# Optimization experiments

Hardware: AMD Instinct MI355X
Metric: run time of the kernel (lower is better)

## Reference

```python
import jax, jax.numpy as jnp
import numpy as np

N_NODES = 50000
D_IN = 128
D_OUT = 128
N_EDGES = 800000


def setup_inputs() -> dict:
    key = jax.random.key(0)
    k1, k2, k3, k4 = jax.random.split(key, 4)
    x = jax.random.normal(k1, (N_NODES, D_IN), dtype=jnp.float32)
    # nn.Linear(input_size, output_size, bias=False): weight is [out, in], y = x @ W.T.
    # We store W1 as [in, out] so y = x @ W1 (same math, transposed storage).
    W1 = jax.random.normal(k2, (D_IN, D_OUT), dtype=jnp.float32) * (1.0 / np.sqrt(D_IN))
    row = jax.random.randint(k3, (N_EDGES,), 0, N_NODES, dtype=jnp.int64)
    col = jax.random.randint(k4, (N_EDGES,), 0, N_NODES, dtype=jnp.int64)
    edge_index = jnp.stack([row, col], axis=0)  # [2, E]
    return {"x": x, "W1": W1, "edge_index": edge_index}


def reference(x, W1, edge_index):
    # Linear transform: [N, D_in] @ [D_in, D_out] -> [N, D_out]
    norm_m = x @ W1
    adj_row = edge_index[0]  # source nodes (gather)
    adj_col = edge_index[1]  # destination nodes (scatter)
    gathered = norm_m[adj_row]  # [E, D_out]
    pooled = jax.ops.segment_max(gathered, adj_col, num_segments=x.shape[0])
    # torch_scatter fills segments with no incoming edges with 0 (not -inf)
    deg = jax.ops.segment_sum(jnp.ones_like(adj_col, dtype=jnp.int32), adj_col,
                              num_segments=x.shape[0])
    pooled = jnp.where((deg > 0)[:, None], pooled, jnp.zeros_like(pooled))
    return jnp.concatenate((x, pooled), axis=1)  # [N, D_in + D_out]
```

## Files before the change

### kernel.cpp

```cpp
#include <hip/hip_runtime.h>


#define N_DIN 128
#define CAP 64

typedef __attribute__((ext_vector_type(8))) short bf16x8;
typedef __attribute__((ext_vector_type(4))) float f32x4;

__device__ __forceinline__ short f32_bf16(float f) {
    unsigned u = __float_as_uint(f);
    return (short)((u + 0x7fffu + ((u >> 16) & 1u)) >> 16);
}

__global__ __launch_bounds__(256) void wconv(const float* __restrict__ W,
                                             short* __restrict__ Wt) {
    int i = blockIdx.x * 256 + threadIdx.x;
    int k = i >> 5, n0 = (i & 31) * 4;
    float4 v = *(const float4*)(W + k * 128 + n0);
    Wt[(n0 + 0) * 128 + k] = f32_bf16(v.x);
    Wt[(n0 + 1) * 128 + k] = f32_bf16(v.y);
    Wt[(n0 + 2) * 128 + k] = f32_bf16(v.z);
    Wt[(n0 + 3) * 128 + k] = f32_bf16(v.w);
}

__global__ __launch_bounds__(256) void fused_gemm_scatter(
        const float* __restrict__ X, const short* __restrict__ Wt,
        short* __restrict__ Yb, float* __restrict__ out, int N, int gblocks,
        const int* __restrict__ row, const int* __restrict__ col,
        int* __restrict__ cur, unsigned short* __restrict__ csrc, int E) {
    if ((int)blockIdx.x >= gblocks) {
        int e = ((int)blockIdx.x - gblocks) * 256 + (int)threadIdx.x;
        if (e < E) {
            int dst = col[e];
            int pos = atomicAdd(&cur[dst], 1);
            if (pos < CAP)
                csrc[dst * CAP + pos] = (unsigned short)row[e];
        }
        return;
    }
    __shared__ short c_lds[4][32][128];
    const int tid = threadIdx.x;
    const int w = tid >> 6, l = tid & 63;
    const int lr = l & 15, lg = l >> 4;
    const int R0 = (int)blockIdx.x * 128 + w * 32;

    bf16x8 af[2][4];
#pragma unroll
    for (int rt = 0; rt < 2; ++rt) {
        int gr = R0 + rt * 16 + lr;
        int grc = gr < N ? gr : N - 1;
#pragma unroll
        for (int t = 0; t < 4; ++t) {
            int kc = t * 32 + lg * 8;
            float4 v0 = *(const float4*)(X + (size_t)grc * 128 + kc);
            float4 v1 = *(const float4*)(X + (size_t)grc * 128 + kc + 4);
            if (gr < N) {
                *(float4*)(out + (size_t)gr * 256 + kc)     = v0;
                *(float4*)(out + (size_t)gr * 256 + kc + 4) = v1;
            }
            bf16x8 a;
            a[0] = f32_bf16(v0.x); a[1] = f32_bf16(v0.y);
            a[2] = f32_bf16(v0.z); a[3] = f32_bf16(v0.w);
            a[4] = f32_bf16(v1.x); a[5] = f32_bf16(v1.y);
            a[6] = f32_bf16(v1.z); a[7] = f32_bf16(v1.w);
            af[rt][t] = a;
        }
    }
#pragma unroll
    for (int ct = 0; ct < 8; ++ct) {
        f32x4 c0 = {0.f, 0.f, 0.f, 0.f}, c1 = {0.f, 0.f, 0.f, 0.f};
        const short* bp = Wt + (ct * 16 + lr) * 128;
#pragma unroll
        for (int t = 0; t < 4; ++t) {
            bf16x8 b = *(const bf16x8*)(bp + t * 32 + lg * 8);
            c0 = __builtin_amdgcn_mfma_f32_16x16x32_bf16(af[0][t], b, c0, 0, 0, 0);
            c1 = __builtin_amdgcn_mfma_f32_16x16x32_bf16(af[1][t], b, c1, 0, 0, 0);
        }
#pragma unroll
        for (int i = 0; i < 4; ++i) {
            c_lds[w][lg * 4 + i][ct * 16 + lr]      = f32_bf16(c0[i]);
            c_lds[w][16 + lg * 4 + i][ct * 16 + lr] = f32_bf16(c1[i]);
        }
    }
#pragma unroll
    for (int it = 0; it < 8; ++it) {
        int cid = it * 64 + l;
        int r2 = cid >> 4, c2 = cid & 15;
        int gr = R0 + r2;
        if (gr < N) {
            bf16x8 vv = *(const bf16x8*)(&c_lds[w][r2][c2 * 8]);
            *(bf16x8*)(Yb + (size_t)gr * 128 + c2 * 8) = vv;
        }
    }
}

__global__ __launch_bounds__(256) void pool_bf16(const unsigned* __restrict__ nmb,
                                                 const int* __restrict__ cur,
                                                 const unsigned short* __restrict__ csrc,
                                                 float* __restrict__ out, int N) {
    int node = blockIdx.x * 4 + (threadIdx.x >> 6);
    if (node >= N) return;
    int lane = threadIdx.x & 63;
    int deg = cur[node];
    if (deg > CAP) deg = CAP;
    const unsigned short* lst = csrc + node * CAP;
    float2 acc = make_float2(-INFINITY, -INFINITY);
    int j = 0;
    for (; j + 4 <= deg; j += 4) {
        int s0 = lst[j], s1 = lst[j + 1], s2 = lst[j + 2], s3 = lst[j + 3];
        unsigned v0 = nmb[s0 * 64 + lane];
        unsigned v1 = nmb[s1 * 64 + lane];
        unsigned v2 = nmb[s2 * 64 + lane];
        unsigned v3 = nmb[s3 * 64 + lane];
        acc.x = fmaxf(acc.x, fmaxf(fmaxf(__uint_as_float(v0 << 16), __uint_as_float(v1 << 16)),
                                   fmaxf(__uint_as_float(v2 << 16), __uint_as_float(v3 << 16))));
        acc.y = fmaxf(acc.y, fmaxf(fmaxf(__uint_as_float(v0 & 0xffff0000u), __uint_as_float(v1 & 0xffff0000u)),
                                   fmaxf(__uint_as_float(v2 & 0xffff0000u), __uint_as_float(v3 & 0xffff0000u))));
    }
    for (; j < deg; ++j) {
        unsigned v0 = nmb[lst[j] * 64 + lane];
        acc.x = fmaxf(acc.x, __uint_as_float(v0 << 16));
        acc.y = fmaxf(acc.y, __uint_as_float(v0 & 0xffff0000u));
    }
    if (deg == 0) acc = make_float2(0.f, 0.f);
    *(float2*)(out + (size_t)node * 256 + N_DIN + lane * 2) = acc;
}

extern "C" void kernel_launch(void* const* d_in, const int* in_sizes, int n_in,
                              void* d_out, int out_size, void* d_ws, size_t ws_size,
                              hipStream_t stream) {
    const float* x  = (const float*)d_in[0];
    const float* W1 = (const float*)d_in[1];
    const int* ei   = (const int*)d_in[2];
    const int N = in_sizes[0] / N_DIN;
    const int E = in_sizes[2] / 2;
    const int* row = ei;
    const int* col = ei + E;
    float* out = (float*)d_out;

    short* norm_mb = (short*)d_ws;
    short* Wt = norm_mb + (size_t)N * N_DIN;
    int* cur  = (int*)(Wt + 128 * 128);
    unsigned short* csrc = (unsigned short*)(cur + N);

    const int gblocks = (N + 127) / 128;
    const int sblocks = (E + 255) / 256;

    hipMemsetAsync(cur, 0, (size_t)N * sizeof(int), stream);
    wconv<<<16, 256, 0, stream>>>(W1, Wt);
    fused_gemm_scatter<<<gblocks + sblocks, 256, 0, stream>>>(
        x, Wt, norm_mb, out, N, gblocks, row, col, cur, csrc, E);
    pool_bf16<<<(N + 3) / 4, 256, 0, stream>>>((const unsigned*)norm_mb, cur, csrc, out, N);
}
```

Before: 168.6 us.

## Merge memset, weight convert, GEMM/scatter and pooling into one cooperative kernel

Replaces the memset plus three kernel launches with a single persistent cooperative kernel. Grid-wide syncs separate the weight conversion and counter clearing, the GEMM/edge-bucketing phase, and the max-pooling phase. The aim is to remove launch gaps and inter-kernel drain between stages. In exchange, a persistent grid sized by occupancy replaces the many small blocks, adds grid-barrier cost, and keeps the original multi-kernel path as a fallback if the cooperative launch fails.

```diff
diff --git a/kernel.cpp b/kernel.cpp
--- a/kernel.cpp
+++ b/kernel.cpp
@@ -1,4 +1,7 @@
 #include <hip/hip_runtime.h>
+#include <hip/hip_cooperative_groups.h>
+
+namespace cg = cooperative_groups;
 
 
 #define N_DIN 128
@@ -12,9 +15,8 @@
     return (short)((u + 0x7fffu + ((u >> 16) & 1u)) >> 16);
 }
 
-__global__ __launch_bounds__(256) void wconv(const float* __restrict__ W,
-                                             short* __restrict__ Wt) {
-    int i = blockIdx.x * 256 + threadIdx.x;
+__device__ __forceinline__ void wconv_unit(int i, const float* __restrict__ W,
+                                           short* __restrict__ Wt) {
     int k = i >> 5, n0 = (i & 31) * 4;
     float4 v = *(const float4*)(W + k * 128 + n0);
     Wt[(n0 + 0) * 128 + k] = f32_bf16(v.x);
@@ -23,26 +25,14 @@
     Wt[(n0 + 3) * 128 + k] = f32_bf16(v.w);
 }
 
-__global__ __launch_bounds__(256) void fused_gemm_scatter(
-        const float* __restrict__ X, const short* __restrict__ Wt,
-        short* __restrict__ Yb, float* __restrict__ out, int N, int gblocks,
-        const int* __restrict__ row, const int* __restrict__ col,
-        int* __restrict__ cur, unsigned short* __restrict__ csrc, int E) {
-    if ((int)blockIdx.x >= gblocks) {
-        int e = ((int)blockIdx.x - gblocks) * 256 + (int)threadIdx.x;
-        if (e < E) {
-            int dst = col[e];
-            int pos = atomicAdd(&cur[dst], 1);
-            if (pos < CAP)
-                csrc[dst * CAP + pos] = (unsigned short)row[e];
-        }
-        return;
-    }
-    __shared__ short c_lds[4][32][128];
-    const int tid = threadIdx.x;
+__device__ __forceinline__ void gemm_tile(int tile, const float* __restrict__ X,
+                                          const short* __restrict__ Wt,
+                                          short* __restrict__ Yb,
+                                          float* __restrict__ out, int N, int tid,
+                                          short (*c_lds)[32][128]) {
     const int w = tid >> 6, l = tid & 63;
     const int lr = l & 15, lg = l >> 4;
-    const int R0 = (int)blockIdx.x * 128 + w * 32;
+    const int R0 = tile * 128 + w * 32;
 
     bf16x8 af[2][4];
 #pragma unroll
@@ -94,13 +84,11 @@
     }
 }
 
-__global__ __launch_bounds__(256) void pool_bf16(const unsigned* __restrict__ nmb,
-                                                 const int* __restrict__ cur,
-                                                 const unsigned short* __restrict__ csrc,
-                                                 float* __restrict__ out, int N) {
-    int node = blockIdx.x * 4 + (threadIdx.x >> 6);
-    if (node >= N) return;
-    int lane = threadIdx.x & 63;
+__device__ __forceinline__ void pool_node(int node, int lane,
+                                          const unsigned* __restrict__ nmb,
+                                          const int* __restrict__ cur,
+                                          const unsigned short* __restrict__ csrc,
+                                          float* __restrict__ out) {
     int deg = cur[node];
     if (deg > CAP) deg = CAP;
     const unsigned short* lst = csrc + node * CAP;
@@ -126,14 +114,100 @@
     *(float2*)(out + (size_t)node * 256 + N_DIN + lane * 2) = acc;
 }
 
+__global__ __launch_bounds__(256) void mega(const float* __restrict__ X,
+                                            const float* __restrict__ W,
+                                            short* __restrict__ Wt,
+                                            short* __restrict__ Yb,
+                                            float* __restrict__ out,
+                                            int* __restrict__ cur,
+                                            unsigned short* __restrict__ csrc,
+                                            const int* __restrict__ row,
+                                            const int* __restrict__ col,
+                                            int N, int E) {
+    __shared__ short c_lds[4][32][128];
+    cg::grid_group g = cg::this_grid();
+    const int tid = threadIdx.x;
+    const int bid = blockIdx.x;
+    const int nb  = gridDim.x;
+
+    {
+        int i = bid * 256 + tid;
+        if (i < 4096) wconv_unit(i, W, Wt);
+        for (int j = i; j < N; j += nb * 256) cur[j] = 0;
+    }
+    __threadfence();
+    g.sync();
+    __threadfence();
+
+    const int gunits = (N + 127) >> 7;
+    const int sunits = (E + 255) >> 8;
+    for (int u = bid; u < gunits + sunits; u += nb) {
+        if (u < gunits) {
+            gemm_tile(u, X, Wt, Yb, out, N, tid, c_lds);
+        } else {
+            int e = (u - gunits) * 256 + tid;
+            if (e < E) {
+                int dst = col[e];
+                int pos = atomicAdd(&cur[dst], 1);
+                if (pos < CAP) csrc[dst * CAP + pos] = (unsigned short)row[e];
+            }
+        }
+    }
+    __threadfence();
+    g.sync();
+    __threadfence();
+
+    const int w = tid >> 6, lane = tid & 63;
+    const int punits = (N + 3) >> 2;
+    for (int u = bid; u < punits; u += nb) {
+        int node = u * 4 + w;
+        if (node < N) pool_node(node, lane, (const unsigned*)Yb, cur, csrc, out);
+    }
+}
+
+__global__ __launch_bounds__(256) void wconv_k(const float* __restrict__ W,
+                                               short* __restrict__ Wt) {
+    int i = blockIdx.x * 256 + threadIdx.x;
+    if (i < 4096) wconv_unit(i, W, Wt);
+}
+
+__global__ __launch_bounds__(256) void fused_k(const float* __restrict__ X,
+                                               const short* __restrict__ Wt,
+                                               short* __restrict__ Yb,
+                                               float* __restrict__ out, int N, int gblocks,
+                                               const int* __restrict__ row,
+                                               const int* __restrict__ col,
+                                               int* __restrict__ cur,
+                                               unsigned short* __restrict__ csrc, int E) {
+    __shared__ short c_lds[4][32][128];
+    if ((int)blockIdx.x >= gblocks) {
+        int e = ((int)blockIdx.x - gblocks) * 256 + (int)threadIdx.x;
+        if (e < E) {
+            int dst = col[e];
+            int pos = atomicAdd(&cur[dst], 1);
+            if (pos < CAP) csrc[dst * CAP + pos] = (unsigned short)row[e];
+        }
+        return;
+    }
+    gemm_tile(blockIdx.x, X, Wt, Yb, out, N, threadIdx.x, c_lds);
+}
+
+__global__ __launch_bounds__(256) void pool_k(const unsigned* __restrict__ nmb,
+                                              const int* __restrict__ cur,
+                                              const unsigned short* __restrict__ csrc,
+                                              float* __restrict__ out, int N) {
+    int node = blockIdx.x * 4 + (threadIdx.x >> 6);
+    if (node < N) pool_node(node, threadIdx.x & 63, nmb, cur, csrc, out);
+}
+
 extern "C" void kernel_launch(void* const* d_in, const int* in_sizes, int n_in,
                               void* d_out, int out_size, void* d_ws, size_t ws_size,
                               hipStream_t stream) {
     const float* x  = (const float*)d_in[0];
     const float* W1 = (const float*)d_in[1];
     const int* ei   = (const int*)d_in[2];
-    const int N = in_sizes[0] / N_DIN;
-    const int E = in_sizes[2] / 2;
+    int N = in_sizes[0] / N_DIN;
+    int E = in_sizes[2] / 2;
     const int* row = ei;
     const int* col = ei + E;
     float* out = (float*)d_out;
@@ -143,12 +217,26 @@
     int* cur  = (int*)(Wt + 128 * 128);
     unsigned short* csrc = (unsigned short*)(cur + N);
 
-    const int gblocks = (N + 127) / 128;
-    const int sblocks = (E + 255) / 256;
-
-    hipMemsetAsync(cur, 0, (size_t)N * sizeof(int), stream);
-    wconv<<<16, 256, 0, stream>>>(W1, Wt);
-    fused_gemm_scatter<<<gblocks + sblocks, 256, 0, stream>>>(
-        x, Wt, norm_mb, out, N, gblocks, row, col, cur, csrc, E);
-    pool_bf16<<<(N + 3) / 4, 256, 0, stream>>>((const unsigned*)norm_mb, cur, csrc, out, N);
-}
+    int maxb = 0;
+    hipError_t oe = hipOccupancyMaxActiveBlocksPerMultiprocessor(&maxb, mega, 256, 0);
+    int grid = (oe == hipSuccess && maxb > 0) ? maxb * 256 : 0;
+    if (grid > 2048) grid = 2048;
+
+    hipError_t err = hipErrorUnknown;
+    if (grid > 0) {
+        void* args[] = { (void*)&x, (void*)&W1, (void*)&Wt, (void*)&norm_mb,
+                         (void*)&out, (void*)&cur, (void*)&csrc,
+                         (void*)&row, (void*)&col, (void*)&N, (void*)&E };
+        err = hipLaunchCooperativeKernel(mega, dim3(grid), dim3(256), args, 0, stream);
+    }
+    if (err != hipSuccess) {
+        (void)hipGetLastError();
+        const int gblocks = (N + 127) / 128;
+        const int sblocks = (E + 255) / 256;
+        hipMemsetAsync(cur, 0, (size_t)N * sizeof(int), stream);
+        wconv_k<<<16, 256, 0, stream>>>(W1, Wt);
+        fused_k<<<gblocks + sblocks, 256, 0, stream>>>(x, Wt, norm_mb, out, N, gblocks,
+                                                       row, col, cur, csrc, E);
+        pool_k<<<(N + 3) / 4, 256, 0, stream>>>((const unsigned*)norm_mb, cur, csrc, out, N);
+    }
+}
```

Result: slower. 480.2 us (+184.8%).
